# Kernel optimization log

Measured on AMD Instinct MI355X. Metric: run time of the kernel, lower is better.

## Reference

```python
import jax, jax.numpy as jnp
import numpy as np

H, W = 320, 320
HID = 64


def setup_inputs() -> dict:
    key = jax.random.key(0)
    k1, k2, k3 = jax.random.split(key, 3)
    K = jnp.array([[300.0, 0.0, 160.0], [0.0, 300.0, 160.0], [0.0, 0.0, 1.0]], jnp.float32)
    t_world_cam = jnp.array([[1.0, 0.0, 0.0, 0.0], [0.0, 1.0, 0.0, 0.0], [0.0, 0.0, 1.0, -2.5], [0.0, 0.0, 0.0, 1.0]], jnp.float32)
    return {
        'K': K,
        't_world_cam': t_world_cam,
        'aabb_min': -jnp.ones(3, jnp.float32),
        'aabb_max': jnp.ones(3, jnp.float32),
        'W1': jax.random.normal(k1, (3, HID), jnp.float32) * 0.5,
        'b1': jnp.zeros(HID, jnp.float32),
        'W2': jax.random.normal(k2, (HID, HID), jnp.float32) * (1.0 / np.sqrt(HID)),
        'b2': jnp.zeros(HID, jnp.float32),
        'W3': jax.random.normal(k3, (HID, 4), jnp.float32) * (1.0 / np.sqrt(HID)),
        'b3': jnp.zeros(4, jnp.float32),
        'n_samples': 32,
    }


def reference(K, t_world_cam, aabb_min, aabb_max, W1, b1, W2, b2, W3, b3, n_samples):
    dt = K.dtype
    # --- world rays (View.world_rays) ---
    fx, fy, cx, cy = K[0, 0], K[1, 1], K[0, 2], K[1, 2]
    u = jnp.arange(W, dtype=dt) + 0.5
    v = jnp.arange(H, dtype=dt) + 0.5
    vv, uu = jnp.meshgrid(v, u, indexing='ij')  # (H,W)
    d = jnp.stack([(uu - cx) / fx, (vv - cy) / fy, jnp.ones_like(uu)], -1)
    d = d / jnp.linalg.norm(d, axis=-1, keepdims=True)          # (H,W,3) view dirs
    R = t_world_cam[:3, :3]
    d = d.reshape(-1, 3) @ R.T                                   # (N,3) world dirs
    o = jnp.broadcast_to(t_world_cam[:3, 3], d.shape)            # (N,3) world origins
    # --- ray/AABB slab intersection ---
    inv = 1.0 / d
    t1 = (aabb_min - o) * inv
    t2 = (aabb_max - o) * inv
    tnear = jnp.max(jnp.minimum(t1, t2), -1)
    tfar = jnp.min(jnp.maximum(t1, t2), -1)
    hit = tnear < tfar
    tn = jnp.where(hit, tnear, 0.0)
    tf = jnp.where(hit, tfar, 1.0)
    # --- uniform sampling along rays ---
    frac = (jnp.arange(n_samples, dtype=dt) + 0.5) / n_samples
    ts = tn[:, None] + (tf - tn)[:, None] * frac                 # (N,S)
    xyz = o[:, None] + ts[..., None] * d[:, None]                # (N,S,3)
    nxyz = (xyz - aabb_min) / (aabb_max - aabb_min) * 2.0 - 1.0  # normalize to [-1,1]
    # --- radiance field MLP ---
    h = jax.nn.relu(nxyz @ W1 + b1)
    h = jax.nn.relu(h @ W2 + b2)
    raw = h @ W3 + b3                                            # (N,S,4)
    sigma = jax.nn.softplus(raw[..., 0])                         # (N,S)
    color = jax.nn.sigmoid(raw[..., 1:])                         # (N,S,3)
    # --- integrate_path: volumetric alpha compositing ---
    delta = jnp.concatenate([jnp.diff(ts, axis=-1), tf[:, None] - ts[:, -1:]], -1)
    sa = sigma * delta
    sa_cum = jnp.cumsum(sa, -1)
    T_prev = jnp.exp(-(sa_cum - sa))                             # transmittance before sample
    weights = T_prev * (1.0 - jnp.exp(-sa))
    rgb = jnp.einsum('ns,nsc->nc', weights, color)               # (N,3)
    alpha = 1.0 - jnp.exp(-sa_cum[:, -1])                        # 1 - T at ray exit
    rgb = jnp.where(hit[:, None], rgb, 0.0)
    alpha = jnp.where(hit, alpha, 0.0)
    img = jnp.concatenate([rgb, alpha[:, None]], -1).reshape(H, W, 4)
    return jnp.transpose(img, (2, 0, 1))                         # (4,H,W)
```

## Files before the change

### kernel.cpp

```cpp
#include <hip/hip_runtime.h>
#include <hip/hip_bf16.h>

#define IMG_H 320
#define IMG_W 320
#define NPIX (IMG_H * IMG_W)
#define HID 64
#define NS 32

typedef __attribute__((ext_vector_type(8))) short short8;
typedef __attribute__((ext_vector_type(4))) float float4v;
typedef __attribute__((ext_vector_type(4))) int   int4v;

#define W2T_OFF 0
#define W1T_OFF 4096
#define W3T_OFF (4096 + 2048)
#define B3P_FLT ((4096 + 2048 + 1024) / 2)

__device__ __forceinline__ unsigned f2bf(float f) {
    __hip_bfloat16 b = __float2bfloat16(f);
    return (unsigned)*reinterpret_cast<unsigned short*>(&b);
}

__device__ __forceinline__ unsigned cvtpk(float lo, float hi) {
    unsigned r;
    asm("v_cvt_pk_bf16_f32 %0, %1, %2" : "=v"(r) : "v"(lo), "v"(hi));
    return r;
}

__device__ __forceinline__ short8 packfrag(float4v lo, float4v hi) {
    int4v p;
    p[0] = (int)cvtpk(fmaxf(lo[0], 0.f), fmaxf(lo[1], 0.f));
    p[1] = (int)cvtpk(fmaxf(lo[2], 0.f), fmaxf(lo[3], 0.f));
    p[2] = (int)cvtpk(fmaxf(hi[0], 0.f), fmaxf(hi[1], 0.f));
    p[3] = (int)cvtpk(fmaxf(hi[2], 0.f), fmaxf(hi[3], 0.f));
    return *reinterpret_cast<short8*>(&p);
}

template <int CTRL, int RMASK>
__device__ __forceinline__ float dppadd(float x) {
    int s = __builtin_amdgcn_update_dpp(0, __float_as_int(x), CTRL, RMASK, 0xF, true);
    return x + __int_as_float(s);
}
__device__ __forceinline__ float scan32(float x) {
    x = dppadd<0x111, 0xF>(x);
    x = dppadd<0x112, 0xF>(x);
    x = dppadd<0x114, 0xF>(x);
    x = dppadd<0x118, 0xF>(x);
    x = dppadd<0x142, 0xA>(x);
    return x;
}

__global__ __launch_bounds__(256) void prep(const float* __restrict__ W1,
                                            const float* __restrict__ b1,
                                            const float* __restrict__ W2,
                                            const float* __restrict__ W3,
                                            const float* __restrict__ b3,
                                            short* __restrict__ wsS) {
    int t = threadIdx.x;
    float* wsF = reinterpret_cast<float*>(wsS);
    for (int i = t; i < 4096; i += 256) {
        int idx = i >> 9, m = (i >> 5) & 15, k2 = i & 31;
        int j3 = 32 * (idx >> 2) + 8 * (m >> 2) + 4 * ((idx >> 1) & 1) + (m & 3);
        int k  = 32 * (idx & 1) + k2;
        wsS[W2T_OFF + i] = (short)f2bf(W2[k * HID + j3]);
    }
    for (int i = t; i < 2048; i += 256) {
        int tt = i >> 9, m = (i >> 5) & 15, k = i & 31;
        int j = 32 * (tt >> 1) + 8 * (m >> 2) + 4 * (tt & 1) + (m & 3);
        float v = (k < 3) ? W1[k * HID + j] : ((k == 3) ? b1[j] : 0.0f);
        wsS[W1T_OFF + i] = (short)f2bf(v);
    }
    for (int i = t; i < 1024; i += 256) {
        int c = i >> 6, j = i & 63;
        float v = (c < 4) ? W3[j * 4 + c] : 0.0f;
        wsS[W3T_OFF + i] = (short)f2bf(v);
    }
    if (t < 16) wsF[B3P_FLT + t] = (t < 4) ? b3[t] : 0.0f;
}

__global__ __launch_bounds__(256, 2) void nerf_reg(
    const float* __restrict__ Kmat, const float* __restrict__ Twc,
    const float* __restrict__ aabb_min, const float* __restrict__ aabb_max,
    const short* __restrict__ ws, const float* __restrict__ b2,
    float* __restrict__ out) {
    __shared__ float rawLds[4][256];

    const int tid  = threadIdx.x;
    const int wave = tid >> 6;
    const int lane = tid & 63;
    const int l15  = lane & 15;
    const int g    = lane >> 4;

    const short* w2t = ws + W2T_OFF;
    const short* w1t = ws + W1T_OFF;
    const short* w3t = ws + W3T_OFF;
    const float* b3p = reinterpret_cast<const float*>(ws) + B3P_FLT;
    float* rawf = rawLds[wave];

    const int sampleId = blockIdx.x * 256 + tid;
    const int pix = sampleId >> 5;
    const int s   = sampleId & 31;

    int y = pix / IMG_W, x = pix - y * IMG_W;
    float fx = Kmat[0], cx = Kmat[2], fy = Kmat[4], cy = Kmat[5];
    float u = (float)x + 0.5f, v = (float)y + 0.5f;
    float dcx = (u - cx) * __builtin_amdgcn_rcpf(fx);
    float dcy = (v - cy) * __builtin_amdgcn_rcpf(fy);
    float dcz = 1.0f;
    float inorm = rsqrtf(dcx * dcx + dcy * dcy + dcz * dcz);
    dcx *= inorm; dcy *= inorm; dcz *= inorm;
    float dx = Twc[0] * dcx + Twc[1] * dcy + Twc[2]  * dcz;
    float dy = Twc[4] * dcx + Twc[5] * dcy + Twc[6]  * dcz;
    float dz = Twc[8] * dcx + Twc[9] * dcy + Twc[10] * dcz;
    float ox = Twc[3], oy = Twc[7], oz = Twc[11];

    float mnx = aabb_min[0], mny = aabb_min[1], mnz = aabb_min[2];
    float mxx = aabb_max[0], mxy = aabb_max[1], mxz = aabb_max[2];
    float ivx = __builtin_amdgcn_rcpf(dx);
    float ivy = __builtin_amdgcn_rcpf(dy);
    float ivz = __builtin_amdgcn_rcpf(dz);
    float t1x = (mnx - ox) * ivx, t2x = (mxx - ox) * ivx;
    float t1y = (mny - oy) * ivy, t2y = (mxy - oy) * ivy;
    float t1z = (mnz - oz) * ivz, t2z = (mxz - oz) * ivz;
    float tnear = fmaxf(fmaxf(fminf(t1x, t2x), fminf(t1y, t2y)), fminf(t1z, t2z));
    float tfar  = fminf(fminf(fmaxf(t1x, t2x), fmaxf(t1y, t2y)), fmaxf(t1z, t2z));
    bool hit = tnear < tfar;
    float tn = hit ? tnear : 0.0f;
    float tf = hit ? tfar  : 1.0f;
    float step = (tf - tn) * (1.0f / NS);
    float ts = tn + (tf - tn) * (((float)s + 0.5f) * (1.0f / NS));
    float px = ox + ts * dx, py = oy + ts * dy, pz = oz + ts * dz;
    float iex = __builtin_amdgcn_rcpf(mxx - mnx);
    float iey = __builtin_amdgcn_rcpf(mxy - mny);
    float iez = __builtin_amdgcn_rcpf(mxz - mnz);
    float nx = fmaf(px - mnx, 2.0f * iex, -1.0f);
    float ny = fmaf(py - mny, 2.0f * iey, -1.0f);
    float nz = fmaf(pz - mnz, 2.0f * iez, -1.0f);

    unsigned pd0 = cvtpk(nx, ny);
    unsigned pd1 = cvtpk(nz, 1.0f);

    short8 a1[4];
#pragma unroll
    for (int t = 0; t < 4; ++t)
        a1[t] = *reinterpret_cast<const short8*>(w1t + (t * 16 + l15) * 32 + 8 * g);
    short8 a2[8];
#pragma unroll
    for (int i = 0; i < 8; ++i)
        a2[i] = *reinterpret_cast<const short8*>(w2t + (i * 16 + l15) * 32 + 8 * g);
    short8 a3[2];
#pragma unroll
    for (int T3 = 0; T3 < 2; ++T3)
        a3[T3] = *reinterpret_cast<const short8*>(w3t + l15 * HID + 32 * T3 + 8 * g);
    float4v binit[4];
#pragma unroll
    for (int uu = 0; uu < 4; ++uu)
        binit[uu] = *reinterpret_cast<const float4v*>(
            b2 + 32 * (uu >> 1) + 4 * (uu & 1) + 8 * g);
    float4v ci = *reinterpret_cast<const float4v*>(b3p + 4 * g);

#pragma unroll
    for (int nt = 0; nt < 4; ++nt) {
        int u0 = __shfl((int)pd0, 16 * nt + l15, 64);
        int u1 = __shfl((int)pd1, 16 * nt + l15, 64);
        int4v bi;
        bi[0] = (g == 0) ? u0 : 0;
        bi[1] = (g == 0) ? u1 : 0;
        bi[2] = 0; bi[3] = 0;
        short8 bx = *reinterpret_cast<short8*>(&bi);

        float4v c1[4];
#pragma unroll
        for (int t = 0; t < 4; ++t)
            c1[t] = __builtin_amdgcn_mfma_f32_16x16x32_bf16(
                a1[t], bx, (float4v){0.f, 0.f, 0.f, 0.f}, 0, 0, 0);
        short8 pa0 = packfrag(c1[0], c1[1]);
        short8 pa1 = packfrag(c1[2], c1[3]);

        float4v c2[4];
#pragma unroll
        for (int uu = 0; uu < 4; ++uu) c2[uu] = binit[uu];
#pragma unroll
        for (int uu = 0; uu < 4; ++uu)
            c2[uu] = __builtin_amdgcn_mfma_f32_16x16x32_bf16(a2[uu * 2 + 0], pa0,
                                                             c2[uu], 0, 0, 0);
#pragma unroll
        for (int uu = 0; uu < 4; ++uu)
            c2[uu] = __builtin_amdgcn_mfma_f32_16x16x32_bf16(a2[uu * 2 + 1], pa1,
                                                             c2[uu], 0, 0, 0);
        short8 pb0 = packfrag(c2[0], c2[1]);
        short8 pb1 = packfrag(c2[2], c2[3]);

        float4v dv = __builtin_amdgcn_mfma_f32_16x16x32_bf16(a3[0], pb0, ci, 0, 0, 0);
        dv = __builtin_amdgcn_mfma_f32_16x16x32_bf16(a3[1], pb1, dv, 0, 0, 0);
        if (g == 0)
            *reinterpret_cast<float4v*>(rawf + (16 * nt + l15) * 4) = dv;
    }
    asm volatile("s_waitcnt lgkmcnt(0)" ::: "memory");

    float4v raw = *reinterpret_cast<const float4v*>(rawf + lane * 4);
    float r0 = raw[0], r1 = raw[1], r2 = raw[2], r3 = raw[3];

    float sigma = fmaxf(r0, 0.0f) + __logf(1.0f + __expf(-fabsf(r0)));
    float c0 = __builtin_amdgcn_rcpf(1.0f + __expf(-r1));
    float c1 = __builtin_amdgcn_rcpf(1.0f + __expf(-r2));
    float c2 = __builtin_amdgcn_rcpf(1.0f + __expf(-r3));
    float delta = (s == NS - 1) ? 0.5f * step : step;
    float sa = sigma * delta;

    float cum = scan32(sa);
    float Tprev = __expf(-(cum - sa));
    float w = Tprev * (1.0f - __expf(-sa));
    float rr = scan32(w * c0);
    float rg = scan32(w * c1);
    float rb = scan32(w * c2);

    if (s == NS - 1) {
        float alpha = 1.0f - __expf(-cum);
        float o0 = rr, o1 = rg, o2 = rb;
        if (!hit) { o0 = 0.0f; o1 = 0.0f; o2 = 0.0f; alpha = 0.0f; }
        out[0 * NPIX + pix] = o0;
        out[1 * NPIX + pix] = o1;
        out[2 * NPIX + pix] = o2;
        out[3 * NPIX + pix] = alpha;
    }
}

extern "C" void kernel_launch(void* const* d_in, const int* in_sizes, int n_in,
                              void* d_out, int out_size, void* d_ws, size_t ws_size,
                              hipStream_t stream) {
    const float* Kmat = (const float*)d_in[0];
    const float* Twc  = (const float*)d_in[1];
    const float* amn  = (const float*)d_in[2];
    const float* amx  = (const float*)d_in[3];
    const float* W1   = (const float*)d_in[4];
    const float* b1   = (const float*)d_in[5];
    const float* W2   = (const float*)d_in[6];
    const float* b2   = (const float*)d_in[7];
    const float* W3   = (const float*)d_in[8];
    const float* b3   = (const float*)d_in[9];
    float* out = (float*)d_out;
    short* ws  = (short*)d_ws;

    prep<<<1, 256, 0, stream>>>(W1, b1, W2, W3, b3, ws);

    int blocks = NPIX * NS / 256;
    nerf_reg<<<blocks, 256, 0, stream>>>(Kmat, Twc, amn, amx, ws, b2, out);
}
```

Before: 74.73 us.

## Stage packed weights in LDS via async loads and compute ray setup once per pixel

Each block now copies the packed bf16 weights and biases (b2 moved into the workspace) into shared memory with global_load_lds, and the per-thread fragment loads read from LDS instead of global/L2. Ray generation and AABB intersection run once per pixel on 8 threads, which write compact per-ray coefficients to shared memory. Every sample thread then derives its normalized position with three FMAs. This removes redundant per-sample ray math and repeated global weight reads, at the cost of about 15 KB of extra LDS per block and a block-wide barrier.

```diff
diff --git a/kernel.cpp b/kernel.cpp
--- a/kernel.cpp
+++ b/kernel.cpp
@@ -14,7 +14,9 @@
 #define W2T_OFF 0
 #define W1T_OFF 4096
 #define W3T_OFF (4096 + 2048)
-#define B3P_FLT ((4096 + 2048 + 1024) / 2)
+#define B3P_FLT 3584
+#define B2_FLT  3600
+#define WS_BYTES 15360
 
 __device__ __forceinline__ unsigned f2bf(float f) {
     __hip_bfloat16 b = __float2bfloat16(f);
@@ -50,11 +52,18 @@
     return x;
 }
 
+__device__ __forceinline__ void gload_lds16(const void* g, void* l) {
+    __builtin_amdgcn_global_load_lds(
+        (const __attribute__((address_space(1))) unsigned int*)g,
+        (__attribute__((address_space(3))) unsigned int*)l, 16, 0, 0);
+}
+
 __global__ __launch_bounds__(256) void prep(const float* __restrict__ W1,
                                             const float* __restrict__ b1,
                                             const float* __restrict__ W2,
                                             const float* __restrict__ W3,
                                             const float* __restrict__ b3,
+                                            const float* __restrict__ b2,
                                             short* __restrict__ wsS) {
     int t = threadIdx.x;
     float* wsF = reinterpret_cast<float*>(wsS);
@@ -76,14 +85,18 @@
         wsS[W3T_OFF + i] = (short)f2bf(v);
     }
     if (t < 16) wsF[B3P_FLT + t] = (t < 4) ? b3[t] : 0.0f;
-}
-
-__global__ __launch_bounds__(256, 2) void nerf_reg(
+    if (t < 64) wsF[B2_FLT + t] = b2[t];
+    for (int i = t; i < (WS_BYTES / 4) - (B2_FLT + 64); i += 256)
+        wsF[B2_FLT + 64 + i] = 0.0f;
+}
+
+__global__ __launch_bounds__(256, 2) void nerf_reg2(
     const float* __restrict__ Kmat, const float* __restrict__ Twc,
     const float* __restrict__ aabb_min, const float* __restrict__ aabb_max,
-    const short* __restrict__ ws, const float* __restrict__ b2,
-    float* __restrict__ out) {
-    __shared__ float rawLds[4][256];
+    const short* __restrict__ ws, float* __restrict__ out) {
+    __shared__ __align__(16) short wlds[WS_BYTES / 2];
+    __shared__ __align__(16) float pp[8][12];
+    __shared__ __align__(16) float rawLds[4][256];
 
     const int tid  = threadIdx.x;
     const int wave = tid >> 6;
@@ -91,51 +104,74 @@
     const int l15  = lane & 15;
     const int g    = lane >> 4;
 
-    const short* w2t = ws + W2T_OFF;
-    const short* w1t = ws + W1T_OFF;
-    const short* w3t = ws + W3T_OFF;
-    const float* b3p = reinterpret_cast<const float*>(ws) + B3P_FLT;
+    {
+        const char* wsb = (const char*)ws;
+        char* wl = (char*)wlds;
+        for (int c = wave; c < WS_BYTES / 1024; c += 4)
+            gload_lds16(wsb + c * 1024 + lane * 16, wl + c * 1024);
+    }
+
+    if (tid < 8) {
+        int p = blockIdx.x * 8 + tid;
+        int y = p / IMG_W, x = p - y * IMG_W;
+        float fx = Kmat[0], cx = Kmat[2], fy = Kmat[4], cy = Kmat[5];
+        float u = (float)x + 0.5f, v = (float)y + 0.5f;
+        float dcx = (u - cx) * __builtin_amdgcn_rcpf(fx);
+        float dcy = (v - cy) * __builtin_amdgcn_rcpf(fy);
+        float dcz = 1.0f;
+        float inorm = rsqrtf(dcx * dcx + dcy * dcy + dcz * dcz);
+        dcx *= inorm; dcy *= inorm; dcz *= inorm;
+        float dx = Twc[0] * dcx + Twc[1] * dcy + Twc[2]  * dcz;
+        float dy = Twc[4] * dcx + Twc[5] * dcy + Twc[6]  * dcz;
+        float dz = Twc[8] * dcx + Twc[9] * dcy + Twc[10] * dcz;
+        float ox = Twc[3], oy = Twc[7], oz = Twc[11];
+
+        float mnx = aabb_min[0], mny = aabb_min[1], mnz = aabb_min[2];
+        float mxx = aabb_max[0], mxy = aabb_max[1], mxz = aabb_max[2];
+        float ivx = __builtin_amdgcn_rcpf(dx);
+        float ivy = __builtin_amdgcn_rcpf(dy);
+        float ivz = __builtin_amdgcn_rcpf(dz);
+        float t1x = (mnx - ox) * ivx, t2x = (mxx - ox) * ivx;
+        float t1y = (mny - oy) * ivy, t2y = (mxy - oy) * ivy;
+        float t1z = (mnz - oz) * ivz, t2z = (mxz - oz) * ivz;
+        float tnear = fmaxf(fmaxf(fminf(t1x, t2x), fminf(t1y, t2y)), fminf(t1z, t2z));
+        float tfar  = fminf(fminf(fmaxf(t1x, t2x), fmaxf(t1y, t2y)), fmaxf(t1z, t2z));
+        bool hit = tnear < tfar;
+        float tn = hit ? tnear : 0.0f;
+        float tf = hit ? tfar  : 1.0f;
+        float step = (tf - tn) * (1.0f / NS);
+        float iex = 2.0f * __builtin_amdgcn_rcpf(mxx - mnx);
+        float iey = 2.0f * __builtin_amdgcn_rcpf(mxy - mny);
+        float iez = 2.0f * __builtin_amdgcn_rcpf(mxz - mnz);
+        pp[tid][0] = dx * iex;
+        pp[tid][1] = dy * iey;
+        pp[tid][2] = dz * iez;
+        pp[tid][3] = (ox - mnx) * iex - 1.0f;
+        pp[tid][4] = (oy - mny) * iey - 1.0f;
+        pp[tid][5] = (oz - mnz) * iez - 1.0f;
+        pp[tid][6] = tn;
+        pp[tid][7] = step;
+        pp[tid][8] = hit ? 1.0f : 0.0f;
+    }
+    __syncthreads();
+
+    const short* w2l = wlds + W2T_OFF;
+    const short* w1l = wlds + W1T_OFF;
+    const short* w3l = wlds + W3T_OFF;
+    const float* bpf = reinterpret_cast<const float*>(wlds);
     float* rawf = rawLds[wave];
 
-    const int sampleId = blockIdx.x * 256 + tid;
-    const int pix = sampleId >> 5;
-    const int s   = sampleId & 31;
-
-    int y = pix / IMG_W, x = pix - y * IMG_W;
-    float fx = Kmat[0], cx = Kmat[2], fy = Kmat[4], cy = Kmat[5];
-    float u = (float)x + 0.5f, v = (float)y + 0.5f;
-    float dcx = (u - cx) * __builtin_amdgcn_rcpf(fx);
-    float dcy = (v - cy) * __builtin_amdgcn_rcpf(fy);
-    float dcz = 1.0f;
-    float inorm = rsqrtf(dcx * dcx + dcy * dcy + dcz * dcz);
-    dcx *= inorm; dcy *= inorm; dcz *= inorm;
-    float dx = Twc[0] * dcx + Twc[1] * dcy + Twc[2]  * dcz;
-    float dy = Twc[4] * dcx + Twc[5] * dcy + Twc[6]  * dcz;
-    float dz = Twc[8] * dcx + Twc[9] * dcy + Twc[10] * dcz;
-    float ox = Twc[3], oy = Twc[7], oz = Twc[11];
-
-    float mnx = aabb_min[0], mny = aabb_min[1], mnz = aabb_min[2];
-    float mxx = aabb_max[0], mxy = aabb_max[1], mxz = aabb_max[2];
-    float ivx = __builtin_amdgcn_rcpf(dx);
-    float ivy = __builtin_amdgcn_rcpf(dy);
-    float ivz = __builtin_amdgcn_rcpf(dz);
-    float t1x = (mnx - ox) * ivx, t2x = (mxx - ox) * ivx;
-    float t1y = (mny - oy) * ivy, t2y = (mxy - oy) * ivy;
-    float t1z = (mnz - oz) * ivz, t2z = (mxz - oz) * ivz;
-    float tnear = fmaxf(fmaxf(fminf(t1x, t2x), fminf(t1y, t2y)), fminf(t1z, t2z));
-    float tfar  = fminf(fminf(fmaxf(t1x, t2x), fmaxf(t1y, t2y)), fmaxf(t1z, t2z));
-    bool hit = tnear < tfar;
-    float tn = hit ? tnear : 0.0f;
-    float tf = hit ? tfar  : 1.0f;
-    float step = (tf - tn) * (1.0f / NS);
-    float ts = tn + (tf - tn) * (((float)s + 0.5f) * (1.0f / NS));
-    float px = ox + ts * dx, py = oy + ts * dy, pz = oz + ts * dz;
-    float iex = __builtin_amdgcn_rcpf(mxx - mnx);
-    float iey = __builtin_amdgcn_rcpf(mxy - mny);
-    float iez = __builtin_amdgcn_rcpf(mxz - mnz);
-    float nx = fmaf(px - mnx, 2.0f * iex, -1.0f);
-    float ny = fmaf(py - mny, 2.0f * iey, -1.0f);
-    float nz = fmaf(pz - mnz, 2.0f * iez, -1.0f);
+    const int s  = tid & 31;
+    const int lp = (tid >> 5) & 7;
+
+    float4v P0 = *reinterpret_cast<const float4v*>(&pp[lp][0]);
+    float4v P1 = *reinterpret_cast<const float4v*>(&pp[lp][4]);
+    float hitf = pp[lp][8];
+    float step = P1[3];
+    float tsv  = fmaf(step, (float)s + 0.5f, P1[2]);
+    float nx = fmaf(tsv, P0[0], P0[3]);
+    float ny = fmaf(tsv, P0[1], P1[0]);
+    float nz = fmaf(tsv, P0[2], P1[1]);
 
     unsigned pd0 = cvtpk(nx, ny);
     unsigned pd1 = cvtpk(nz, 1.0f);
@@ -143,21 +179,21 @@
     short8 a1[4];
 #pragma unroll
     for (int t = 0; t < 4; ++t)
-        a1[t] = *reinterpret_cast<const short8*>(w1t + (t * 16 + l15) * 32 + 8 * g);
+        a1[t] = *reinterpret_cast<const short8*>(w1l + (t * 16 + l15) * 32 + 8 * g);
     short8 a2[8];
 #pragma unroll
     for (int i = 0; i < 8; ++i)
-        a2[i] = *reinterpret_cast<const short8*>(w2t + (i * 16 + l15) * 32 + 8 * g);
+        a2[i] = *reinterpret_cast<const short8*>(w2l + (i * 16 + l15) * 32 + 8 * g);
     short8 a3[2];
 #pragma unroll
     for (int T3 = 0; T3 < 2; ++T3)
-        a3[T3] = *reinterpret_cast<const short8*>(w3t + l15 * HID + 32 * T3 + 8 * g);
+        a3[T3] = *reinterpret_cast<const short8*>(w3l + l15 * HID + 32 * T3 + 8 * g);
     float4v binit[4];
 #pragma unroll
     for (int uu = 0; uu < 4; ++uu)
         binit[uu] = *reinterpret_cast<const float4v*>(
-            b2 + 32 * (uu >> 1) + 4 * (uu & 1) + 8 * g);
-    float4v ci = *reinterpret_cast<const float4v*>(b3p + 4 * g);
+            bpf + B2_FLT + 32 * (uu >> 1) + 4 * (uu & 1) + 8 * g);
+    float4v ci = *reinterpret_cast<const float4v*>(bpf + B3P_FLT + 4 * g);
 
 #pragma unroll
     for (int nt = 0; nt < 4; ++nt) {
@@ -216,9 +252,10 @@
     float rb = scan32(w * c2);
 
     if (s == NS - 1) {
+        int pix = blockIdx.x * 8 + lp;
         float alpha = 1.0f - __expf(-cum);
         float o0 = rr, o1 = rg, o2 = rb;
-        if (!hit) { o0 = 0.0f; o1 = 0.0f; o2 = 0.0f; alpha = 0.0f; }
+        if (hitf == 0.0f) { o0 = 0.0f; o1 = 0.0f; o2 = 0.0f; alpha = 0.0f; }
         out[0 * NPIX + pix] = o0;
         out[1 * NPIX + pix] = o1;
         out[2 * NPIX + pix] = o2;
@@ -242,8 +279,8 @@
     float* out = (float*)d_out;
     short* ws  = (short*)d_ws;
 
-    prep<<<1, 256, 0, stream>>>(W1, b1, W2, W3, b3, ws);
+    prep<<<1, 256, 0, stream>>>(W1, b1, W2, W3, b3, b2, ws);
 
     int blocks = NPIX * NS / 256;
-    nerf_reg<<<blocks, 256, 0, stream>>>(Kmat, Twc, amn, amx, ws, b2, out);
-}
+    nerf_reg2<<<blocks, 256, 0, stream>>>(Kmat, Twc, amn, amx, ws, out);
+}
```

Result: faster. 70.23 us (-6.0%).
